# Kernel tuning notes

Hardware: AMD Instinct MI355X
Metric: run time of the kernel (lower is better)

Reference implementation:

```python
import jax, jax.numpy as jnp
import numpy as np

D_MODEL = 1024
N_HEADS = 16
HEAD_DIM = D_MODEL // N_HEADS
ROPE_BASE = 10000.0


def rope_rot(t, pos):
    # t: [B, L, H, hd], pos: [L] int32 absolute positions. Rotate-half RoPE.
    hd = t.shape[-1]
    inv_freq = 1.0 / (ROPE_BASE ** (jnp.arange(0, hd, 2, dtype=jnp.float32) / hd))
    freqs = pos.astype(jnp.float32)[:, None] * inv_freq[None, :]  # [L, hd/2]
    cos = jnp.cos(freqs)[None, :, None, :]  # [1, L, 1, hd/2]
    sin = jnp.sin(freqs)[None, :, None, :]
    t1, t2 = t[..., : hd // 2], t[..., hd // 2 :]
    return jnp.concatenate([t1 * cos - t2 * sin, t2 * cos + t1 * sin], axis=-1)


def setup_inputs() -> dict:
    key = jax.random.key(0)
    ks = jax.random.split(key, 8)
    B, L, S = 8, 16, 8192
    x = jax.random.normal(ks[0], (B, L, D_MODEL), dtype=jnp.float32)
    cache_k = jax.random.normal(ks[1], (B, S, N_HEADS, HEAD_DIM), dtype=jnp.float32)
    cache_v = jax.random.normal(ks[2], (B, S, N_HEADS, HEAD_DIM), dtype=jnp.float32)
    sc = 1.0 / np.sqrt(D_MODEL)
    qkv_w = jax.random.normal(ks[3], (D_MODEL, 3 * D_MODEL), dtype=jnp.float32) * sc
    qkv_b = jnp.zeros((3 * D_MODEL,), dtype=jnp.float32)
    o_w = jax.random.normal(ks[4], (D_MODEL, D_MODEL), dtype=jnp.float32) * sc
    o_b = jnp.zeros((D_MODEL,), dtype=jnp.float32)
    return {
        "x": x,
        "cache_k": cache_k,
        "cache_v": cache_v,
        "qkv_w": qkv_w,
        "qkv_b": qkv_b,
        "o_w": o_w,
        "o_b": o_b,
        "cache_index": S,
    }


def reference(x, cache_k, cache_v, qkv_w, qkv_b, o_w, o_b, cache_index):
    B, L, _ = x.shape
    qkv = x @ qkv_w + qkv_b  # [B, L, 3*d]
    q, k, v = jnp.split(qkv, 3, axis=-1)
    q = q.reshape(B, L, N_HEADS, HEAD_DIM)
    k = k.reshape(B, L, N_HEADS, HEAD_DIM)
    v = v.reshape(B, L, N_HEADS, HEAD_DIM)
    pos = cache_index + jnp.arange(L, dtype=jnp.int32)
    q = rope_rot(q, pos)
    k = rope_rot(k, pos)
    # streaming: append new k/v to cache (cached entries already RoPE-rotated)
    k_full = jnp.concatenate([cache_k, k], axis=1)  # [B, S+L, H, hd]
    v_full = jnp.concatenate([cache_v, v], axis=1)
    scale = 1.0 / jnp.sqrt(jnp.asarray(HEAD_DIM, dtype=q.dtype))
    scores = jnp.einsum("blhd,bshd->bhls", q, k_full) * scale  # [B, H, L, S+L]
    probs = jax.nn.softmax(scores, axis=-1)  # no mask in original module
    out = jnp.einsum("bhls,bshd->blhd", probs, v_full)
    out = out.reshape(B, L, D_MODEL)
    return out @ o_w + o_b
```

## Files before the change

kernel.cpp:

```cpp
#include <hip/hip_runtime.h>

#define B_ 8
#define L_ 16
#define H_ 16
#define D_ 64
#define DM 1024
#define S_ 8192

__device__ __forceinline__ void gld_lds16(const float* g, float* l) {
  __builtin_amdgcn_global_load_lds(
      (const __attribute__((address_space(1))) void*)g,
      (__attribute__((address_space(3))) void*)l, 16, 0, 0);
}

__global__ void __launch_bounds__(256) gemm_splitk_kernel(
    const float* __restrict__ A, const float* __restrict__ W,
    float* __restrict__ part, int lda, int ldw, int Kchunk)
{
  const int c0 = blockIdx.x * 64;
  const int k0 = blockIdx.y * Kchunk;
  const int t  = threadIdx.x;
  __shared__ float xs[32][132];
  __shared__ float wsm[32][64];
  float acc[8][4];
  #pragma unroll
  for (int i = 0; i < 8; ++i)
    #pragma unroll
    for (int j = 0; j < 4; ++j) acc[i][j] = 0.f;
  const int rg = t >> 4, cg = t & 15;
  const int r0 = rg * 8, ct0 = cg * 4;
  for (int ks = 0; ks < Kchunk; ks += 32) {
    __syncthreads();
    #pragma unroll
    for (int i = 0; i < 4; ++i) {
      int fi = t + i * 256;
      int r = fi >> 3, kq = fi & 7;
      float4 v = *(const float4*)(A + (size_t)r * lda + k0 + ks + kq * 4);
      xs[kq*4+0][r] = v.x; xs[kq*4+1][r] = v.y;
      xs[kq*4+2][r] = v.z; xs[kq*4+3][r] = v.w;
    }
    #pragma unroll
    for (int i = 0; i < 2; ++i) {
      int si = t + i * 256;
      int kk = si >> 4, cq = si & 15;
      *(float4*)&wsm[kk][cq*4] =
          *(const float4*)(W + (size_t)(k0 + ks + kk) * ldw + c0 + cq * 4);
    }
    __syncthreads();
    #pragma unroll
    for (int kk = 0; kk < 32; ++kk) {
      float a[8], bb[4];
      *(float4*)&a[0] = *(const float4*)&xs[kk][r0];
      *(float4*)&a[4] = *(const float4*)&xs[kk][r0 + 4];
      *(float4*)&bb[0] = *(const float4*)&wsm[kk][ct0];
      #pragma unroll
      for (int ii = 0; ii < 8; ++ii)
        #pragma unroll
        for (int jj = 0; jj < 4; ++jj)
          acc[ii][jj] = fmaf(a[ii], bb[jj], acc[ii][jj]);
    }
  }
  float* po = part + (size_t)blockIdx.y * 128 * ldw;
  #pragma unroll
  for (int ii = 0; ii < 8; ++ii)
    #pragma unroll
    for (int jj = 0; jj < 4; ++jj)
      po[(size_t)(r0 + ii) * ldw + c0 + ct0 + jj] = acc[ii][jj];
}

__global__ void ropefuse_kernel(const float* __restrict__ part,
                                const float* __restrict__ bias,
                                const int* __restrict__ cidx,
                                float* __restrict__ qh, float* __restrict__ kn,
                                float* __restrict__ vn)
{
  int gt = blockIdx.x * 256 + threadIdx.x;
  int i = gt & 31, l = (gt >> 5) & 15, h = (gt >> 9) & 15, b = gt >> 13;
  int row = b * L_ + l;
  const int PS = 128 * 3072;
  const float* pr = part + (size_t)row * 3072;
  int cq = h * 64 + i;
  int cols[6] = {cq, cq + 32, 1024 + cq, 1024 + cq + 32, 2048 + cq, 2048 + cq + 32};
  float v[6];
  #pragma unroll
  for (int c = 0; c < 6; ++c) {
    float s = bias[cols[c]];
    #pragma unroll
    for (int ks = 0; ks < 4; ++ks) s += pr[(size_t)ks * PS + cols[c]];
    v[c] = s;
  }
  int pos = cidx[0] + l;
  float inv = exp2f((float)i * (-13.287712379549449f / 32.0f));
  float fr = (float)pos * inv;
  float sn, cs;
  sincosf(fr, &sn, &cs);
  int ob = ((b * H_ + h) * L_ + l) * 64;
  qh[ob + i]      = (v[0] * cs - v[1] * sn) * 0.125f;
  qh[ob + 32 + i] = (v[1] * cs + v[0] * sn) * 0.125f;
  kn[ob + i]      = v[2] * cs - v[3] * sn;
  kn[ob + 32 + i] = v[3] * cs + v[2] * sn;
  vn[ob + i]      = v[4];
  vn[ob + 32 + i] = v[5];
}

__global__ void __launch_bounds__(512, 4) attn_partial_kernel(
    const float* __restrict__ qh, const float* __restrict__ kc,
    const float* __restrict__ vc, float* __restrict__ opart,
    float* __restrict__ lpart)
{
  const int chunk = blockIdx.x;
  const int b     = blockIdx.y;
  const int tid   = threadIdx.x;
  const int w = tid >> 6, lane = tid & 63;
  const int h = tid >> 5, l = (tid >> 1) & 15, dh = tid & 1;
  __shared__ float kv[2][8192];

  float4 qr[8];
  {
    const float* qb = qh + (size_t)b * 16384 + (size_t)tid * 32;
    #pragma unroll
    for (int j = 0; j < 8; ++j)
      qr[j] = *(const float4*)(qb + ((j ^ (dh << 2)) << 2));
  }
  float4 o[8];
  #pragma unroll
  for (int j = 0; j < 8; ++j) o[j].x = o[j].y = o[j].z = o[j].w = 0.f;
  float l_run = 0.f;

  const size_t kbase = (size_t)b * S_ * DM;
  const int st0 = chunk * 128;

  auto issue = [&](int t, int buf) {
    const int r = st0 + t * 4 + (w & 3);
    const float* src = (w < 4 ? kc : vc) + kbase + (size_t)r * DM + lane * 4;
    float* dst = &kv[buf][(w < 4 ? 0 : 4096) + (w & 3) * 1024];
    #pragma unroll
    for (int i = 0; i < 4; ++i)
      gld_lds16(src + i * 256, dst + i * 256);
  };

  issue(0, 0);
  asm volatile("s_waitcnt vmcnt(0)" ::: "memory");
  __syncthreads();

  const int koff = h * 64 + dh * 32;
  for (int t = 0; t < 32; ++t) {
    const int cb = t & 1;
    if (t < 31) {
      issue(t + 1, cb ^ 1);
      asm volatile("s_waitcnt vmcnt(4)" ::: "memory");
    } else {
      asm volatile("s_waitcnt vmcnt(0)" ::: "memory");
    }
    __builtin_amdgcn_sched_barrier(0);
    __builtin_amdgcn_s_barrier();

    #pragma unroll
    for (int r = 0; r < 4; ++r) {
      const float* kr = &kv[cb][r * 1024 + koff];
      const float* vr = &kv[cb][4096 + r * 1024 + koff];
      float sc = 0.f;
      #pragma unroll
      for (int j = 0; j < 8; ++j) {
        float4 k4 = *(const float4*)(kr + ((j ^ (dh << 2)) << 2));
        sc += k4.x * qr[j].x + k4.y * qr[j].y + k4.z * qr[j].z + k4.w * qr[j].w;
      }
      float s = sc + __shfl_xor(sc, 1);
      float pex = __expf(s);
      l_run += pex;
      #pragma unroll
      for (int j = 0; j < 8; ++j) {
        float4 v4 = *(const float4*)(vr + ((j ^ (dh << 2)) << 2));
        o[j].x = fmaf(pex, v4.x, o[j].x);
        o[j].y = fmaf(pex, v4.y, o[j].y);
        o[j].z = fmaf(pex, v4.z, o[j].z);
        o[j].w = fmaf(pex, v4.w, o[j].w);
      }
    }
    __builtin_amdgcn_s_barrier();
  }

  const size_t ob = (((size_t)(b * 64 + chunk) * 16 + h) * 16 + l) * 64;
  #pragma unroll
  for (int j = 0; j < 8; ++j)
    *(float4*)&opart[ob + dh * 32 + ((j ^ (dh << 2)) << 2)] = o[j];
  if (dh == 0)
    lpart[((b * 64 + chunk) * 16 + h) * 16 + l] = l_run;
}

__global__ void __launch_bounds__(64) combine_kernel(
    const float* __restrict__ qh, const float* __restrict__ kn,
    const float* __restrict__ vn, const float* __restrict__ opart,
    const float* __restrict__ lpart, float* __restrict__ attn)
{
  const int bh = blockIdx.x;
  const int b = bh >> 4, h = bh & 15;
  const int l0 = blockIdx.y * 4;
  const int lane = threadIdx.x;
  __shared__ float kb[1024], vb[1024], qb[256];
  __shared__ float scn[4][16];
  for (int i = 0; i < 16; ++i) {
    kb[i * 64 + lane] = kn[(size_t)(bh * 16 + i) * 64 + lane];
    vb[i * 64 + lane] = vn[(size_t)(bh * 16 + i) * 64 + lane];
  }
  {
    int ll = lane >> 4, sl = lane & 15;
    *(float4*)&qb[ll * 64 + sl * 4] =
        *(const float4*)&qh[(size_t)(bh * 16 + l0 + ll) * 64 + sl * 4];
  }
  __syncthreads();
  {
    int ll = lane >> 4, sp = lane & 15;
    float a = 0.f;
    for (int d = 0; d < 64; ++d) a += qb[ll * 64 + d] * kb[sp * 64 + d];
    scn[ll][sp] = a;
  }
  __syncthreads();
  for (int ll = 0; ll < 4; ++ll) {
    const int l = l0 + ll;
    float den = 0.f, od = 0.f;
    for (int c = 0; c < 64; ++c) {
      den += lpart[((b * 64 + c) * 16 + h) * 16 + l];
      od  += opart[(((size_t)(b * 64 + c) * 16 + h) * 16 + l) * 64 + lane];
    }
    #pragma unroll
    for (int sp = 0; sp < 16; ++sp) {
      float pex = __expf(scn[ll][sp]);
      den += pex;
      od += pex * vb[sp * 64 + lane];
    }
    attn[((size_t)(b * 16 + l) * 16 + h) * 64 + lane] = od / den;
  }
}

__global__ void reduce_out_kernel(const float* __restrict__ part2,
                                  const float* __restrict__ ob,
                                  float* __restrict__ out)
{
  int idx = blockIdx.x * 256 + threadIdx.x;
  int c = idx & 1023;
  float s = ob[c];
  #pragma unroll
  for (int ks = 0; ks < 8; ++ks) s += part2[(size_t)ks * 131072 + idx];
  out[idx] = s;
}

extern "C" void kernel_launch(void* const* d_in, const int* in_sizes, int n_in,
                              void* d_out, int out_size, void* d_ws, size_t ws_size,
                              hipStream_t stream) {
  (void)in_sizes; (void)n_in; (void)out_size; (void)ws_size;
  const float* x       = (const float*)d_in[0];
  const float* cache_k = (const float*)d_in[1];
  const float* cache_v = (const float*)d_in[2];
  const float* qkv_w   = (const float*)d_in[3];
  const float* qkv_b   = (const float*)d_in[4];
  const float* o_w     = (const float*)d_in[5];
  const float* o_b     = (const float*)d_in[6];
  const int*   cidx    = (const int*)d_in[7];
  float* out = (float*)d_out;

  float* ws    = (float*)d_ws;
  float* big   = ws;
  float* part1 = big;
  float* opart = big;
  float* part2 = big;
  float* qh    = big + 8388608;
  float* kn    = qh + 131072;
  float* vn    = kn + 131072;
  float* lpart = vn + 131072;
  float* attn  = lpart + 131072;

  gemm_splitk_kernel<<<dim3(48, 4), 256, 0, stream>>>(x, qkv_w, part1, 1024, 3072, 256);
  ropefuse_kernel<<<256, 256, 0, stream>>>(part1, qkv_b, cidx, qh, kn, vn);
  attn_partial_kernel<<<dim3(64, 8), 512, 0, stream>>>(qh, cache_k, cache_v,
                                                       opart, lpart);
  combine_kernel<<<dim3(128, 4), 64, 0, stream>>>(qh, kn, vn, opart, lpart, attn);
  gemm_splitk_kernel<<<dim3(16, 8), 256, 0, stream>>>(attn, o_w, part2, 1024, 1024, 128);
  reduce_out_kernel<<<512, 256, 0, stream>>>(part2, o_b, out);
}
```

Baseline: 199.7 us.

## Deepen KV streaming pipeline to four smaller LDS stages with one barrier per step

The attention partial kernel's LDS pipeline changes from two 4-row stages to four 2-row stages, with three async global-to-LDS loads kept in flight. Each step now waits, passes one barrier, then issues the next load, which drops the trailing barrier. The goal is to hide more memory latency in this bandwidth-bound KV cache stream. The cost is twice as many barrier and wait points, each covering less compute, and about 64KB of LDS per block, the same as before.

```diff
diff --git a/kernel.cpp b/kernel.cpp
--- a/kernel.cpp
+++ b/kernel.cpp
@@ -112,8 +112,9 @@
   const int b     = blockIdx.y;
   const int tid   = threadIdx.x;
   const int w = tid >> 6, lane = tid & 63;
-  const int h = tid >> 5, l = (tid >> 1) & 15, dh = tid & 1;
-  __shared__ float kv[2][8192];
+  const int h = tid >> 5, dh = tid & 1;
+  const int l = (tid >> 1) & 15;
+  __shared__ float kv[4 * 4096];
 
   float4 qr[8];
   {
@@ -130,55 +131,51 @@
   const size_t kbase = (size_t)b * S_ * DM;
   const int st0 = chunk * 128;
 
-  auto issue = [&](int t, int buf) {
-    const int r = st0 + t * 4 + (w & 3);
-    const float* src = (w < 4 ? kc : vc) + kbase + (size_t)r * DM + lane * 4;
-    float* dst = &kv[buf][(w < 4 ? 0 : 4096) + (w & 3) * 1024];
-    #pragma unroll
-    for (int i = 0; i < 4; ++i)
-      gld_lds16(src + i * 256, dst + i * 256);
+  const float* wsrc0 = (w < 4 ? kc : vc) + kbase + (size_t)(w & 3) * 512 + lane * 4;
+  float* wdst0 = &kv[0] + (w < 4 ? 0 : 2048) + (w & 3) * 512;
+  auto issue = [&](int T) {
+    const float* src = wsrc0 + (size_t)(st0 + T * 2) * DM;
+    float* dst = wdst0 + (T & 3) * 4096;
+    gld_lds16(src, dst);
+    gld_lds16(src + 256, dst + 256);
   };
 
-  issue(0, 0);
-  asm volatile("s_waitcnt vmcnt(0)" ::: "memory");
-  __syncthreads();
+  issue(0); issue(1); issue(2);
 
   const int koff = h * 64 + dh * 32;
-  for (int t = 0; t < 32; ++t) {
-    const int cb = t & 1;
-    if (t < 31) {
-      issue(t + 1, cb ^ 1);
-      asm volatile("s_waitcnt vmcnt(4)" ::: "memory");
-    } else {
-      asm volatile("s_waitcnt vmcnt(0)" ::: "memory");
-    }
-    __builtin_amdgcn_sched_barrier(0);
-    __builtin_amdgcn_s_barrier();
-
-    #pragma unroll
-    for (int r = 0; r < 4; ++r) {
-      const float* kr = &kv[cb][r * 1024 + koff];
-      const float* vr = &kv[cb][4096 + r * 1024 + koff];
-      float sc = 0.f;
-      #pragma unroll
-      for (int j = 0; j < 8; ++j) {
-        float4 k4 = *(const float4*)(kr + ((j ^ (dh << 2)) << 2));
-        sc += k4.x * qr[j].x + k4.y * qr[j].y + k4.z * qr[j].z + k4.w * qr[j].w;
-      }
-      float s = sc + __shfl_xor(sc, 1);
-      float pex = __expf(s);
-      l_run += pex;
-      #pragma unroll
-      for (int j = 0; j < 8; ++j) {
-        float4 v4 = *(const float4*)(vr + ((j ^ (dh << 2)) << 2));
-        o[j].x = fmaf(pex, v4.x, o[j].x);
-        o[j].y = fmaf(pex, v4.y, o[j].y);
-        o[j].z = fmaf(pex, v4.z, o[j].z);
-        o[j].w = fmaf(pex, v4.w, o[j].w);
-      }
-    }
-    __builtin_amdgcn_s_barrier();
-  }
+#define STEP(T, WAITOP) do {                                                  \
+    asm volatile(WAITOP ::: "memory");                                        \
+    __builtin_amdgcn_sched_barrier(0);                                        \
+    __builtin_amdgcn_s_barrier();                                             \
+    if ((T) + 3 < 64) issue((T) + 3);                                         \
+    const float* sb = &kv[((T) & 3) * 4096];                                  \
+    _Pragma("unroll")                                                         \
+    for (int r = 0; r < 2; ++r) {                                             \
+      const float* kr = sb + r * 1024 + koff;                                 \
+      const float* vr = sb + 2048 + r * 1024 + koff;                          \
+      float sc = 0.f;                                                         \
+      _Pragma("unroll")                                                       \
+      for (int j = 0; j < 8; ++j) {                                           \
+        float4 k4 = *(const float4*)(kr + ((j ^ (dh << 2)) << 2));            \
+        sc += k4.x * qr[j].x + k4.y * qr[j].y + k4.z * qr[j].z + k4.w * qr[j].w;\
+      }                                                                       \
+      float s = sc + __shfl_xor(sc, 1);                                       \
+      float pex = __expf(s);                                                  \
+      l_run += pex;                                                           \
+      _Pragma("unroll")                                                       \
+      for (int j = 0; j < 8; ++j) {                                           \
+        float4 v4 = *(const float4*)(vr + ((j ^ (dh << 2)) << 2));            \
+        o[j].x = fmaf(pex, v4.x, o[j].x);                                     \
+        o[j].y = fmaf(pex, v4.y, o[j].y);                                     \
+        o[j].z = fmaf(pex, v4.z, o[j].z);                                     \
+        o[j].w = fmaf(pex, v4.w, o[j].w);                                     \
+      }                                                                       \
+    } } while (0)
+
+  for (int t = 0; t < 62; ++t) STEP(t, "s_waitcnt vmcnt(4)");
+  STEP(62, "s_waitcnt vmcnt(2)");
+  STEP(63, "s_waitcnt vmcnt(0)");
+#undef STEP
 
   const size_t ob = (((size_t)(b * 64 + chunk) * 16 + h) * 16 + l) * 64;
   #pragma unroll
```

After: 208.9 us. 1.05x slower.
